# Kernel optimization log

Measured on AMD Instinct MI355X. Metric: run time of the kernel, lower is better.

Reference implementation:

```python
import jax, jax.numpy as jnp
import numpy as np

A_NUM = 9
C_NUM = 20


def generate_anchor(anc, grid):
    # anc: (A,2) w,h ; grid: (B,H,W,2) centers -> anchors (B,A,H,W,4)
    centers = grid[:, None]                      # (B,1,H,W,2)
    half = anc.reshape(1, -1, 1, 1, 2) * 0.5     # (1,A,1,1,2)
    return jnp.concatenate([centers - half, centers + half], axis=-1)


def iou_matrix(proposals, bboxes):
    # proposals: (B,A,H,W,4) -> (B,K,4); bboxes: (B,N,5)
    B = proposals.shape[0]
    p = proposals.reshape(B, -1, 4)[:, :, None, :]   # (B,K,1,4)
    bb = bboxes[:, None, :, :]                       # (B,1,N,5)
    s_p = (p[..., 2] - p[..., 0]) * (p[..., 3] - p[..., 1])
    s_b = (bb[..., 2] - bb[..., 0]) * (bb[..., 3] - bb[..., 1])
    ix1 = jnp.maximum(p[..., 0], bb[..., 0])
    iy1 = jnp.maximum(p[..., 1], bb[..., 1])
    ix2 = jnp.minimum(p[..., 2], bb[..., 2])
    iy2 = jnp.minimum(p[..., 3], bb[..., 3])
    s_i = jnp.clip(ix2 - ix1, 0.0) * jnp.clip(iy2 - iy1, 0.0)
    s_u = s_p + s_b - s_i
    iou = jnp.clip(s_i / (s_u + 1e-8), 0.0)
    invalid = (s_u <= 0) | (s_p <= 0) | (s_b <= 0) | (bb[..., 0] < 0)
    return jnp.where(invalid, 0.0, iou)              # (B,K,N)


def extract_anchor_data(anchor_data, idx):
    # anchor_data: (B,A,D,H,W) -> flat (B*A*H*W, D) -> gather
    B, A, D, H, W = anchor_data.shape
    flat = jnp.transpose(anchor_data, (0, 1, 3, 4, 2)).reshape(-1, D)
    return flat[idx]


def extract_class_scores(all_scores, idx, num_anchors):
    # all_scores: (B,C,H,W) -> (B,A,H,W,C) flat -> gather
    B, C, H, W = all_scores.shape
    s = jnp.transpose(all_scores, (0, 2, 3, 1))[:, None]          # (B,1,H,W,C)
    s = jnp.broadcast_to(s, (B, num_anchors, H, W, C)).reshape(-1, C)
    return s[idx]


def setup_inputs() -> dict:
    key = jax.random.key(0)
    ks = jax.random.split(key, 8)
    B, Cin, H, W = 32, 1280, 28, 28
    N, M = 64, 4096
    hid, out_ch = 128, 5 * A_NUM + C_NUM
    features = jax.random.normal(ks[0], (B, Cin, H, W), dtype=jnp.float32)
    # grid of feature-cell centers (GenerateGrid-style)
    xs = jnp.arange(W, dtype=jnp.float32) + 0.5
    ys = jnp.arange(H, dtype=jnp.float32) + 0.5
    gx, gy = jnp.meshgrid(xs, ys, indexing='xy')
    grid = jnp.broadcast_to(jnp.stack([gx, gy], axis=-1), (B, H, W, 2))
    anc = jnp.array([[1.0, 1], [2, 2], [3, 3], [4, 4], [5, 5], [2, 3], [3, 2], [3, 5], [5, 3]], dtype=jnp.float32)
    tl = jax.random.uniform(ks[1], (B, N, 2), minval=0.0, maxval=20.0)
    wh = jax.random.uniform(ks[2], (B, N, 2), minval=1.0, maxval=8.0)
    cls = jax.random.randint(ks[3], (B, N, 1), 0, C_NUM).astype(jnp.float32)
    bb = jnp.concatenate([tl, tl + wh, cls], axis=-1)
    valid = jax.random.uniform(ks[4], (B, N, 1)) > 0.25
    bboxes = jnp.where(valid, bb, -1.0)
    K = B * A_NUM * H * W
    pos_anchor_idx = jax.random.randint(ks[5], (M,), 0, K, dtype=jnp.int64 if jax.config.jax_enable_x64 else jnp.int32)
    neg_anchor_idx = jax.random.randint(ks[6], (M,), 0, K, dtype=pos_anchor_idx.dtype)
    W1 = jax.random.normal(ks[7], (hid, Cin), dtype=jnp.float32) * 0.02
    b1 = jnp.zeros((hid,), dtype=jnp.float32)
    W2 = jax.random.normal(jax.random.fold_in(key, 99), (out_ch, hid), dtype=jnp.float32) * 0.02
    b2 = jnp.zeros((out_ch,), dtype=jnp.float32)
    return {"features": features, "grid": grid, "anc": anc, "bboxes": bboxes,
            "pos_anchor_idx": pos_anchor_idx, "neg_anchor_idx": neg_anchor_idx,
            "W1": W1, "b1": b1, "W2": W2, "b2": b2}


def reference(features, grid, anc, bboxes, pos_anchor_idx, neg_anchor_idx, W1, b1, W2, b2):
    B, Cin, H, W = features.shape
    A, C = A_NUM, C_NUM
    # anchors + broadcast IoU matrix
    anchors = generate_anchor(anc, grid)                 # (B,A,H,W,4)
    iou_mat = iou_matrix(anchors, bboxes)                # (B,A*H*W,N)
    # prediction head: 1x1 conv -> (dropout eval: identity) -> leaky_relu -> 1x1 conv
    h = jnp.einsum('bchw,oc->bohw', features, W1) + b1[None, :, None, None]
    h = jax.nn.leaky_relu(h, negative_slope=0.01)
    out = jnp.einsum('bchw,oc->bohw', h, W2) + b2[None, :, None, None]  # (B,5A+C,H,W)
    anchor_raw = out[:, :5 * A].reshape(B, A, 5, H, W)
    conf_sq = jax.nn.sigmoid(anchor_raw[:, :, 0:1])      # (B,A,1,H,W)
    off_raw = anchor_raw[:, :, 1:]                       # (B,A,4,H,W)
    off_sq = jnp.concatenate([jax.nn.sigmoid(off_raw[:, :, :2]) - 0.5, off_raw[:, :, 2:]], axis=2)
    class_raw = out[:, 5 * A:]                           # (B,C,H,W)
    # training path: irregular gathers
    class_scores = extract_class_scores(class_raw, pos_anchor_idx, A)   # (M,C)
    offsets = extract_anchor_data(off_sq, pos_anchor_idx)               # (M,4)
    conf_pos = extract_anchor_data(conf_sq, pos_anchor_idx)             # (M,1)
    conf_neg = extract_anchor_data(conf_sq, neg_anchor_idx)             # (M,1)
    conf_scores = jnp.concatenate([conf_pos, conf_neg], axis=0)         # (2M,1)
    return conf_scores, offsets, class_scores, iou_mat
```

## Files before the change

### kernel.cpp

```cpp
#include <hip/hip_runtime.h>
#include <cstdint>

#define A_NUM 9
#define C_NUM 20
#define B_SZ 32
#define HW 784
#define P_NUM (A_NUM*HW)
#define NBOX 64
#define CIN 1280
#define HID 128
#define M_IDX 4096
#define KS_ALL 40
#define HSF 132
#define OSTR 80
#define IOU_PB 64

#define CONF_OFF 0
#define OFFS_OFF (2*M_IDX)
#define CLS_OFF  (OFFS_OFF + 4*M_IDX)
#define IOU_OFF  (CLS_OFF + C_NUM*M_IDX)

#define GEMM_BLKS 392
#define IOU_BX ((P_NUM + IOU_PB - 1)/IOU_PB)
#define IOU_BLKS (IOU_BX*B_SZ)

typedef short bf16x8 __attribute__((ext_vector_type(8)));
typedef float f32x4  __attribute__((ext_vector_type(4)));

__device__ __forceinline__ unsigned pack_bf16(float lo, float hi) {
  unsigned a = __builtin_bit_cast(unsigned, lo);
  unsigned b = __builtin_bit_cast(unsigned, hi);
  return ((a + 0x8000u) >> 16) | ((b + 0x8000u) & 0xffff0000u);
}

__global__ __launch_bounds__(256) void prep_w(const float* __restrict__ W1,
                                              const float* __restrict__ W2,
                                              uint4* __restrict__ W1f,
                                              uint4* __restrict__ W2f) {
  int id = blockIdx.x * 256 + threadIdx.x;
  if (id < 20480) {
    int lane = id & 63;
    int ntile = (id >> 6) & 7;
    int ks = id >> 9;
    int lo = lane & 15, quad = lane >> 4;
    int n = ntile * 16 + lo;
    int k0 = ks * 32 + quad * 8;
    const float* src = W1 + n * CIN + k0;
    float4 x = *(const float4*)src;
    float4 y = *(const float4*)(src + 4);
    uint4 p;
    p.x = pack_bf16(x.x, x.y);
    p.y = pack_bf16(x.z, x.w);
    p.z = pack_bf16(y.x, y.y);
    p.w = pack_bf16(y.z, y.w);
    W1f[id] = p;
  } else {
    int i2 = id - 20480;
    int lane = i2 & 63;
    int ntile = (i2 >> 6) % 5;
    int ks = i2 / 320;
    int lo = lane & 15, quad = lane >> 4;
    int n = ntile * 16 + lo;
    int k0 = ks * 32 + quad * 8;
    uint4 p = (uint4){0, 0, 0, 0};
    if (n < 5 * A_NUM + C_NUM) {
      const float* src = W2 + n * HID + k0;
      float4 x = *(const float4*)src;
      float4 y = *(const float4*)(src + 4);
      p.x = pack_bf16(x.x, x.y);
      p.y = pack_bf16(x.z, x.w);
      p.z = pack_bf16(y.x, y.y);
      p.w = pack_bf16(y.z, y.w);
    }
    W2f[i2] = p;
  }
}

union SharedU {
  float hs[4][16 * HSF];
  struct { float sb[NBOX * 5]; float4 sp4[IOU_PB]; } i;
};

__global__ __launch_bounds__(256) void fused_main(
    const float* __restrict__ F, const uint4* __restrict__ W1f,
    const uint4* __restrict__ W2f, const float* __restrict__ b1,
    const float* __restrict__ b2, float* __restrict__ Hd,
    const float* __restrict__ gridc, const float* __restrict__ anc,
    const float* __restrict__ bboxes, float* __restrict__ iou_out) {
  __shared__ SharedU sh;
  const int bid = blockIdx.x;
  const int t = threadIdx.x;

  if (bid >= GEMM_BLKS) {
    const int bid2 = bid - GEMM_BLKS;
    const int b = bid2 / IOU_BX;
    const int p0 = (bid2 - b * IOU_BX) * IOU_PB;
    float* sb = sh.i.sb;
    float4* sp4 = sh.i.sp4;
    for (int i = t; i < NBOX * 5; i += 256) sb[i] = bboxes[b * NBOX * 5 + i];
    if (t < IOU_PB) {
      int p = p0 + t;
      float x1 = 0.f, y1 = 0.f, x2 = 0.f, y2 = 0.f;
      if (p < P_NUM) {
        int a = p / HW, hw = p - a * HW;
        float2 c = ((const float2*)gridc)[b * HW + hw];
        float hx = anc[a * 2 + 0] * 0.5f, hy = anc[a * 2 + 1] * 0.5f;
        x1 = c.x - hx; y1 = c.y - hy; x2 = c.x + hx; y2 = c.y + hy;
      }
      sp4[t] = make_float4(x1, y1, x2, y2);
    }
    __syncthreads();
    const int nl = (t & 15) * 4;
    const int pi = t >> 4;
#pragma unroll
    for (int ip = 0; ip < 4; ip++) {
      const int pl = pi + 16 * ip;
      const int p = p0 + pl;
      const float4 pb = sp4[pl];
      const float spA = (pb.z - pb.x) * (pb.w - pb.y);
      float4 res;
#pragma unroll
      for (int jn = 0; jn < 4; jn++) {
        const int n = nl + jn;
        float bx1 = sb[n * 5 + 0], by1 = sb[n * 5 + 1];
        float bx2 = sb[n * 5 + 2], by2 = sb[n * 5 + 3];
        float s_b = (bx2 - bx1) * (by2 - by1);
        float ix1 = fmaxf(pb.x, bx1), iy1 = fmaxf(pb.y, by1);
        float ix2 = fminf(pb.z, bx2), iy2 = fminf(pb.w, by2);
        float si = fmaxf(ix2 - ix1, 0.f) * fmaxf(iy2 - iy1, 0.f);
        float su = spA + s_b - si;
        float iou = fmaxf(si / (su + 1e-8f), 0.f);
        bool invalid = (su <= 0.f) | (spA <= 0.f) | (s_b <= 0.f) | (bx1 < 0.f);
        float v = invalid ? 0.f : iou;
        if (jn == 0) res.x = v; else if (jn == 1) res.y = v;
        else if (jn == 2) res.z = v; else res.w = v;
      }
      if (p < P_NUM)
        *(float4*)&iou_out[((size_t)(b * P_NUM + p)) * 64 + nl] = res;
    }
    return;
  }

  const int w = t >> 6, lane = t & 63;
  const int quad = lane >> 4, lo = lane & 15;
  const int g = bid * 4 + w;
  const int b = g / 49;
  const int mf = g - b * 49;
  const int m0 = mf * 16;

  const float* Fq = F + (size_t)b * CIN * HW + (size_t)quad * 8 * HW + m0 + lo;

  f32x4 acc[8];
#pragma unroll
  for (int i = 0; i < 8; i++) acc[i] = (f32x4){0.f, 0.f, 0.f, 0.f};

  float va0[8], va1[8];
  uint4 vb0[8], vb1[8];

  auto loadA = [&](int kk, float* va) {
    const float* p = Fq + (size_t)kk * 32 * HW;
#pragma unroll
    for (int j = 0; j < 8; j++) va[j] = p[(size_t)j * HW];
  };
  auto loadB = [&](int kk, uint4* vb) {
    const uint4* p = W1f + (size_t)kk * 512 + lane;
#pragma unroll
    for (int nf = 0; nf < 8; nf++) vb[nf] = p[nf * 64];
  };
  auto step = [&](const float* va, const uint4* vb) {
    uint4 ap;
    ap.x = pack_bf16(va[0], va[1]);
    ap.y = pack_bf16(va[2], va[3]);
    ap.z = pack_bf16(va[4], va[5]);
    ap.w = pack_bf16(va[6], va[7]);
    bf16x8 af = __builtin_bit_cast(bf16x8, ap);
#pragma unroll
    for (int nf = 0; nf < 8; nf++)
      acc[nf] = __builtin_amdgcn_mfma_f32_16x16x32_bf16(
          af, __builtin_bit_cast(bf16x8, vb[nf]), acc[nf], 0, 0, 0);
  };

  loadA(0, va0); loadB(0, vb0);
  loadA(1, va1); loadB(1, vb1);
#pragma unroll 2
  for (int kk = 0; kk < KS_ALL; kk += 2) {
    step(va0, vb0);
    if (kk + 2 < KS_ALL) { loadA(kk + 2, va0); loadB(kk + 2, vb0); }
    step(va1, vb1);
    if (kk + 3 < KS_ALL) { loadA(kk + 3, va1); loadB(kk + 3, vb1); }
  }

  {
    float* hsw = sh.hs[w];
#pragma unroll
    for (int nf = 0; nf < 8; nf++) {
      const float bb = b1[nf * 16 + lo];
#pragma unroll
      for (int r = 0; r < 4; r++) {
        float v = acc[nf][r] + bb;
        v = v > 0.f ? v : 0.01f * v;
        hsw[(quad * 4 + r) * HSF + nf * 16 + lo] = v;
      }
    }
  }
  __syncthreads();

  {
    f32x4 acc2[5];
#pragma unroll
    for (int nt = 0; nt < 5; nt++) acc2[nt] = (f32x4){0.f, 0.f, 0.f, 0.f};
    const float* hrow = sh.hs[w] + lo * HSF + quad * 8;
#pragma unroll
    for (int ks = 0; ks < 4; ks++) {
      const float* hp = hrow + ks * 32;
      float2 p0 = *(const float2*)(hp + 0);
      float2 p1 = *(const float2*)(hp + 2);
      float2 p2 = *(const float2*)(hp + 4);
      float2 p3 = *(const float2*)(hp + 6);
      uint4 ap;
      ap.x = pack_bf16(p0.x, p0.y);
      ap.y = pack_bf16(p1.x, p1.y);
      ap.z = pack_bf16(p2.x, p2.y);
      ap.w = pack_bf16(p3.x, p3.y);
      bf16x8 af = __builtin_bit_cast(bf16x8, ap);
#pragma unroll
      for (int nt = 0; nt < 5; nt++) {
        bf16x8 bf = __builtin_bit_cast(bf16x8, W2f[(ks * 5 + nt) * 64 + lane]);
        acc2[nt] = __builtin_amdgcn_mfma_f32_16x16x32_bf16(af, bf, acc2[nt], 0, 0, 0);
      }
    }
    const int mrow = m0 + quad * 4;
#pragma unroll
    for (int nt = 0; nt < 5; nt++) {
      const int o = nt * 16 + lo;
      if (o < 5 * A_NUM + C_NUM) {
        const float bz = b2[o];
        const int t5 = (o < 5 * A_NUM) ? (o % 5) : 5;
#pragma unroll
        for (int r = 0; r < 4; r++) {
          const int m = mrow + r;
          float v = acc2[nt][r] + bz;
          if (t5 == 0) v = 1.f / (1.f + expf(-v));
          else if (t5 == 1 || t5 == 2) v = 1.f / (1.f + expf(-v)) - 0.5f;
          Hd[((size_t)b * HW + m) * OSTR + o] = v;
        }
      }
    }
  }
}

__global__ __launch_bounds__(256) void gather2(
    const int* __restrict__ pos_idx, const int* __restrict__ neg_idx,
    const float* __restrict__ Hd, float* __restrict__ out) {
  const int bid = blockIdx.x;
  if (bid < M_IDX / 8) {
    const int g = threadIdx.x >> 5;
    const int l = threadIdx.x & 31;
    const int slot = bid * 8 + g;
    const int idx = pos_idx[slot];
    const int b = idx / P_NUM, r = idx - b * P_NUM;
    const int a = r / HW, hw = r - a * HW;
    const float* row = Hd + ((size_t)b * HW + hw) * OSTR;
    if (l == 0)       out[CONF_OFF + slot] = row[a * 5];
    else if (l < 5)   out[OFFS_OFF + slot * 4 + (l - 1)] = row[a * 5 + l];
    else if (l < 25)  out[CLS_OFF + slot * C_NUM + (l - 5)] = row[5 * A_NUM + (l - 5)];
  } else {
    const int tt = (bid - M_IDX / 8) * 256 + threadIdx.x;
    if (tt < M_IDX) {
      const int idx = neg_idx[tt];
      const int b = idx / P_NUM, r = idx - b * P_NUM;
      const int a = r / HW, hw = r - a * HW;
      out[CONF_OFF + M_IDX + tt] = Hd[((size_t)b * HW + hw) * OSTR + a * 5];
    }
  }
}

extern "C" void kernel_launch(void* const* d_in, const int* in_sizes, int n_in,
                              void* d_out, int out_size, void* d_ws, size_t ws_size,
                              hipStream_t stream) {
  const float* features = (const float*)d_in[0];
  const float* gridc    = (const float*)d_in[1];
  const float* anc      = (const float*)d_in[2];
  const float* bboxes   = (const float*)d_in[3];
  const int*   pos_idx  = (const int*)d_in[4];
  const int*   neg_idx  = (const int*)d_in[5];
  const float* W1       = (const float*)d_in[6];
  const float* b1       = (const float*)d_in[7];
  const float* W2       = (const float*)d_in[8];
  const float* b2       = (const float*)d_in[9];
  float* out = (float*)d_out;

  uint4* W1f = (uint4*)d_ws;
  uint4* W2f = (uint4*)((char*)d_ws + 327680);
  float* Hd  = (float*)((char*)d_ws + 327680 + 20480);

  hipLaunchKernelGGL(prep_w, dim3(85), dim3(256), 0, stream, W1, W2, W1f, W2f);
  hipLaunchKernelGGL(fused_main, dim3(GEMM_BLKS + IOU_BLKS), dim3(256), 0, stream,
                     features, W1f, W2f, b1, b2, Hd,
                     gridc, anc, bboxes, out + IOU_OFF);
  hipLaunchKernelGGL(gather2, dim3(M_IDX / 8 + 16), dim3(256), 0, stream,
                     pos_idx, neg_idx, Hd, out);
}
```

Baseline: 261.4 us.

## Split GEMM K dimension across four waves with shared-memory reduction

Each block now handles one 16-row M tile, and its four waves each take a quarter of the 1280-wide K range instead of each wave owning a separate M tile over the full K. Partial accumulators are reduced through shared memory. Bias and leaky ReLU are applied there, and the hidden activations are stored as bf16. The second small GEMM is then spread across waves by output tile. The aim is four times more GEMM blocks, for better occupancy and latency hiding, at the cost of extra LDS traffic and two block-wide barriers.

Result: faster. 255.8 us (-2.1%).

```diff
diff --git a/kernel.cpp b/kernel.cpp
--- a/kernel.cpp
+++ b/kernel.cpp
@@ -10,8 +10,8 @@
 #define CIN 1280
 #define HID 128
 #define M_IDX 4096
-#define KS_ALL 40
-#define HSF 132
+#define KS_W 10
+#define HSTR2 136
 #define OSTR 80
 #define IOU_PB 64
 
@@ -20,7 +20,7 @@
 #define CLS_OFF  (OFFS_OFF + 4*M_IDX)
 #define IOU_OFF  (CLS_OFF + C_NUM*M_IDX)
 
-#define GEMM_BLKS 392
+#define GEMM_BLKS (B_SZ*49)
 #define IOU_BX ((P_NUM + IOU_PB - 1)/IOU_PB)
 #define IOU_BLKS (IOU_BX*B_SZ)
 
@@ -77,7 +77,10 @@
 }
 
 union SharedU {
-  float hs[4][16 * HSF];
+  struct {
+    f32x4 red[4][8][64];
+    unsigned short h[16 * HSTR2];
+  } g;
   struct { float sb[NBOX * 5]; float4 sp4[IOU_PB]; } i;
 };
 
@@ -143,12 +146,13 @@
 
   const int w = t >> 6, lane = t & 63;
   const int quad = lane >> 4, lo = lane & 15;
-  const int g = bid * 4 + w;
-  const int b = g / 49;
-  const int mf = g - b * 49;
+  const int b = bid / 49;
+  const int mf = bid - b * 49;
   const int m0 = mf * 16;
 
-  const float* Fq = F + (size_t)b * CIN * HW + (size_t)quad * 8 * HW + m0 + lo;
+  const float* Fq = F + (size_t)b * CIN * HW +
+                    (size_t)(w * (KS_W * 32) + quad * 8) * HW + m0 + lo;
+  const uint4* Wq = W1f + (size_t)(w * KS_W) * 512 + lane;
 
   f32x4 acc[8];
 #pragma unroll
@@ -163,7 +167,7 @@
     for (int j = 0; j < 8; j++) va[j] = p[(size_t)j * HW];
   };
   auto loadB = [&](int kk, uint4* vb) {
-    const uint4* p = W1f + (size_t)kk * 512 + lane;
+    const uint4* p = Wq + (size_t)kk * 512;
 #pragma unroll
     for (int nf = 0; nf < 8; nf++) vb[nf] = p[nf * 64];
   };
@@ -183,55 +187,52 @@
   loadA(0, va0); loadB(0, vb0);
   loadA(1, va1); loadB(1, vb1);
 #pragma unroll 2
-  for (int kk = 0; kk < KS_ALL; kk += 2) {
+  for (int kk = 0; kk < KS_W; kk += 2) {
     step(va0, vb0);
-    if (kk + 2 < KS_ALL) { loadA(kk + 2, va0); loadB(kk + 2, vb0); }
+    if (kk + 2 < KS_W) { loadA(kk + 2, va0); loadB(kk + 2, vb0); }
     step(va1, vb1);
-    if (kk + 3 < KS_ALL) { loadA(kk + 3, va1); loadB(kk + 3, vb1); }
-  }
+    if (kk + 3 < KS_W) { loadA(kk + 3, va1); loadB(kk + 3, vb1); }
+  }
+
+#pragma unroll
+  for (int nf = 0; nf < 8; nf++) sh.g.red[w][nf][lane] = acc[nf];
+  __syncthreads();
+
+#pragma unroll
+  for (int i = 0; i < 2; i++) {
+    const int nf = 2 * w + i;
+    f32x4 s = sh.g.red[0][nf][lane];
+    s += sh.g.red[1][nf][lane];
+    s += sh.g.red[2][nf][lane];
+    s += sh.g.red[3][nf][lane];
+    const float bb = b1[nf * 16 + lo];
+#pragma unroll
+    for (int r = 0; r < 4; r++) {
+      float v = s[r] + bb;
+      v = v > 0.f ? v : 0.01f * v;
+      unsigned u = __builtin_bit_cast(unsigned, v);
+      sh.g.h[(quad * 4 + r) * HSTR2 + nf * 16 + lo] =
+          (unsigned short)((u + 0x8000u) >> 16);
+    }
+  }
+  __syncthreads();
 
   {
-    float* hsw = sh.hs[w];
-#pragma unroll
-    for (int nf = 0; nf < 8; nf++) {
-      const float bb = b1[nf * 16 + lo];
-#pragma unroll
-      for (int r = 0; r < 4; r++) {
-        float v = acc[nf][r] + bb;
-        v = v > 0.f ? v : 0.01f * v;
-        hsw[(quad * 4 + r) * HSF + nf * 16 + lo] = v;
+    bf16x8 af[4];
+#pragma unroll
+    for (int ks = 0; ks < 4; ks++)
+      af[ks] = *(const bf16x8*)(sh.g.h + lo * HSTR2 + ks * 32 + quad * 8);
+    const int mrow = m0 + quad * 4;
+#pragma unroll
+    for (int rep = 0; rep < 2; rep++) {
+      const int nt = rep ? 4 : w;
+      if (rep && w != 0) break;
+      f32x4 acc2 = (f32x4){0.f, 0.f, 0.f, 0.f};
+#pragma unroll
+      for (int ks = 0; ks < 4; ks++) {
+        bf16x8 bf = __builtin_bit_cast(bf16x8, W2f[(ks * 5 + nt) * 64 + lane]);
+        acc2 = __builtin_amdgcn_mfma_f32_16x16x32_bf16(af[ks], bf, acc2, 0, 0, 0);
       }
-    }
-  }
-  __syncthreads();
-
-  {
-    f32x4 acc2[5];
-#pragma unroll
-    for (int nt = 0; nt < 5; nt++) acc2[nt] = (f32x4){0.f, 0.f, 0.f, 0.f};
-    const float* hrow = sh.hs[w] + lo * HSF + quad * 8;
-#pragma unroll
-    for (int ks = 0; ks < 4; ks++) {
-      const float* hp = hrow + ks * 32;
-      float2 p0 = *(const float2*)(hp + 0);
-      float2 p1 = *(const float2*)(hp + 2);
-      float2 p2 = *(const float2*)(hp + 4);
-      float2 p3 = *(const float2*)(hp + 6);
-      uint4 ap;
-      ap.x = pack_bf16(p0.x, p0.y);
-      ap.y = pack_bf16(p1.x, p1.y);
-      ap.z = pack_bf16(p2.x, p2.y);
-      ap.w = pack_bf16(p3.x, p3.y);
-      bf16x8 af = __builtin_bit_cast(bf16x8, ap);
-#pragma unroll
-      for (int nt = 0; nt < 5; nt++) {
-        bf16x8 bf = __builtin_bit_cast(bf16x8, W2f[(ks * 5 + nt) * 64 + lane]);
-        acc2[nt] = __builtin_amdgcn_mfma_f32_16x16x32_bf16(af, bf, acc2[nt], 0, 0, 0);
-      }
-    }
-    const int mrow = m0 + quad * 4;
-#pragma unroll
-    for (int nt = 0; nt < 5; nt++) {
       const int o = nt * 16 + lo;
       if (o < 5 * A_NUM + C_NUM) {
         const float bz = b2[o];
@@ -239,7 +240,7 @@
 #pragma unroll
         for (int r = 0; r < 4; r++) {
           const int m = mrow + r;
-          float v = acc2[nt][r] + bz;
+          float v = acc2[r] + bz;
           if (t5 == 0) v = 1.f / (1.f + expf(-v));
           else if (t5 == 1 || t5 == 2) v = 1.f / (1.f + expf(-v)) - 0.5f;
           Hd[((size_t)b * HW + m) * OSTR + o] = v;
```
